# Kernel tuning notes

Measured on AMD Instinct MI355X. Metric: run time of the kernel, lower is better.

Reference implementation:

```python
import jax, jax.numpy as jnp
import numpy as np
from jax import lax

VOCAB, EMB, HID = 50000, 1024, 1024
H2 = HID // 2            # per-direction LSTM hidden
T = 4096                 # sequence length
NTAGS, START, STOP = 5, 3, 4
NEG = -10000.0


def setup_inputs() -> dict:
    key = jax.random.key(0)
    ks = jax.random.split(key, 16)
    n = lambda i, shape, s=0.05: (jax.random.normal(ks[i], shape) * s).astype(jnp.float32)
    inp = {
        "sentence": jax.random.randint(ks[0], (T,), 0, VOCAB, dtype=jnp.int64 if jax.config.jax_enable_x64 else jnp.int32),
        "h0": jax.random.normal(ks[1], (2, H2), jnp.float32),
        "c0": jax.random.normal(ks[2], (2, H2), jnp.float32),
        "embed": jax.random.normal(ks[3], (VOCAB, EMB), jnp.float32),
        "Wih_f": n(4, (4 * H2, EMB)), "Whh_f": n(5, (4 * H2, H2)),
        "bih_f": n(6, (4 * H2,)),     "bhh_f": n(7, (4 * H2,)),
        "Wih_b": n(8, (4 * H2, EMB)), "Whh_b": n(9, (4 * H2, H2)),
        "bih_b": n(10, (4 * H2,)),    "bhh_b": n(11, (4 * H2,)),
        "Wout": n(12, (NTAGS, HID)),  "bout": n(13, (NTAGS,)),
    }
    trans = jax.random.normal(ks[14], (NTAGS, NTAGS), jnp.float32)
    trans = trans.at[START, :].set(NEG).at[:, STOP].set(NEG)
    inp["trans"] = trans
    return inp


def _lstm_dir(xs, h0, c0, Wih, Whh, bih, bhh):
    # torch LSTM gate order: i, f, g, o
    def step(carry, x):
        h, c = carry
        g = Wih @ x + bih + Whh @ h + bhh
        i, f, gg, o = jnp.split(g, 4)
        c = jax.nn.sigmoid(f) * c + jax.nn.sigmoid(i) * jnp.tanh(gg)
        h = jax.nn.sigmoid(o) * jnp.tanh(c)
        return (h, c), h
    _, hs = lax.scan(step, (h0, c0), xs)
    return hs  # [T, H2]


def reference(sentence, h0, c0, embed,
              Wih_f, Whh_f, bih_f, bhh_f,
              Wih_b, Whh_b, bih_b, bhh_b,
              Wout, bout, trans):
    xs = embed[sentence]  # [T, EMB]
    hf = _lstm_dir(xs, h0[0], c0[0], Wih_f, Whh_f, bih_f, bhh_f)
    hb = _lstm_dir(xs[::-1], h0[1], c0[1], Wih_b, Whh_b, bih_b, bhh_b)[::-1]
    feats = jnp.concatenate([hf, hb], axis=-1) @ Wout.T + bout  # [T, NTAGS]

    # Viterbi decode
    fv0 = jnp.full((NTAGS,), NEG, jnp.float32).at[START].set(0.0)

    def vstep(fv, feat):
        scores = fv[None, :] + trans            # [next_tag, prev_tag]
        bp = jnp.argmax(scores, axis=1)         # best prev for each next
        fv_new = jnp.max(scores, axis=1) + feat
        return fv_new, bp

    fv, bptrs = lax.scan(vstep, fv0, feats)     # bptrs: [T, NTAGS]
    terminal = fv + trans[STOP]
    best = jnp.argmax(terminal)
    path_score = terminal[best]

    def back(tag, bp):
        prev = bp[tag]
        return prev, prev
    _, path_rev = lax.scan(back, best, bptrs[::-1])  # tags at t=T-1..0, last is START
    full = jnp.concatenate([best[None], path_rev])    # length T+1
    best_path = full[::-1][1:]                        # drop START, forward order, length T
    return path_score, best_path
```

## Files before the change

### kernel.cpp

```cpp
#include <hip/hip_runtime.h>
#include <math.h>

#define VOCAB 50000
#define EMB   1024
#define H2    512
#define R4    2048
#define TLEN  4096
#define NTAGS 5
#define STARTT 3
#define STOPT  4
#define NEGV  (-10000.0f)

#define NWG   32
#define SLICE 16

typedef unsigned long long u64;
typedef _Float16 half2v __attribute__((ext_vector_type(2)));

#define ALOAD64(p)    __hip_atomic_load((p), __ATOMIC_RELAXED, __HIP_MEMORY_SCOPE_AGENT)
#define ASTORE64(p,v) __hip_atomic_store((p), (v), __ATOMIC_RELAXED, __HIP_MEMORY_SCOPE_AGENT)

__device__ __forceinline__ float fsig(float x) {
    return __builtin_amdgcn_rcpf(1.f + __expf(-x));
}
__device__ __forceinline__ float ftanh(float x) {
    return 1.f - 2.f * __builtin_amdgcn_rcpf(1.f + __expf(2.f * x));
}

template <int CTRL>
__device__ __forceinline__ float dppadd(float x) {
    int o = __builtin_amdgcn_update_dpp(0, __float_as_int(x), CTRL, 0xf, 0xf, true);
    return x + __int_as_float(o);
}
#define RED16(a) do { \
    a = dppadd<0xB1>(a);    \
    a = dppadd<0x4E>(a);    \
    a = dppadd<0x141>(a);   \
    a = dppadd<0x128>(a);   \
} while (0)

__global__ __launch_bounds__(256) void input_gemm(
    const int* __restrict__ sent, const float* __restrict__ embed,
    const float* __restrict__ WihF, const float* __restrict__ WihB,
    const float* __restrict__ bihF, const float* __restrict__ bhhF,
    const float* __restrict__ bihB, const float* __restrict__ bhhB,
    float* __restrict__ G)
{
    __shared__ float As[32 * 64];
    __shared__ float Bs[32 * 64];
    const int tid = threadIdx.x;
    const int tm = blockIdx.x * 64;
    const int tn = blockIdx.y * 64;
    const int dir = blockIdx.z;
    const float* Wih = dir ? WihB : WihF;

    const int lr = tid >> 2;
    const int lp = tid & 3;
    const int srow = sent[tm + lr];
    const float* arow = embed + (size_t)srow * EMB;
    const float* brow = Wih + (size_t)(tn + lr) * EMB;

    const int mt = (tid & 15) * 4;
    const int nt = (tid >> 4) * 4;
    float acc[4][4] = {};

    for (int k0 = 0; k0 < EMB; k0 += 32) {
        float4 a0 = *(const float4*)(arow + k0 + lp * 8);
        float4 a1 = *(const float4*)(arow + k0 + lp * 8 + 4);
        float4 b0 = *(const float4*)(brow + k0 + lp * 8);
        float4 b1 = *(const float4*)(brow + k0 + lp * 8 + 4);
        __syncthreads();
        const int kb = lp * 8;
        As[(kb + 0) * 64 + lr] = a0.x; As[(kb + 1) * 64 + lr] = a0.y;
        As[(kb + 2) * 64 + lr] = a0.z; As[(kb + 3) * 64 + lr] = a0.w;
        As[(kb + 4) * 64 + lr] = a1.x; As[(kb + 5) * 64 + lr] = a1.y;
        As[(kb + 6) * 64 + lr] = a1.z; As[(kb + 7) * 64 + lr] = a1.w;
        Bs[(kb + 0) * 64 + lr] = b0.x; Bs[(kb + 1) * 64 + lr] = b0.y;
        Bs[(kb + 2) * 64 + lr] = b0.z; Bs[(kb + 3) * 64 + lr] = b0.w;
        Bs[(kb + 4) * 64 + lr] = b1.x; Bs[(kb + 5) * 64 + lr] = b1.y;
        Bs[(kb + 6) * 64 + lr] = b1.z; Bs[(kb + 7) * 64 + lr] = b1.w;
        __syncthreads();
        #pragma unroll
        for (int k = 0; k < 32; ++k) {
            float4 av = *(const float4*)(As + k * 64 + mt);
            float4 bv = *(const float4*)(Bs + k * 64 + nt);
            acc[0][0] += av.x * bv.x; acc[0][1] += av.x * bv.y; acc[0][2] += av.x * bv.z; acc[0][3] += av.x * bv.w;
            acc[1][0] += av.y * bv.x; acc[1][1] += av.y * bv.y; acc[1][2] += av.y * bv.z; acc[1][3] += av.y * bv.w;
            acc[2][0] += av.z * bv.x; acc[2][1] += av.z * bv.y; acc[2][2] += av.z * bv.z; acc[2][3] += av.z * bv.w;
            acc[3][0] += av.w * bv.x; acc[3][1] += av.w * bv.y; acc[3][2] += av.w * bv.z; acc[3][3] += av.w * bv.w;
        }
    }

    const float* bih = dir ? bihB : bihF;
    const float* bhh = dir ? bhhB : bhhF;
    float bias[4];
    #pragma unroll
    for (int jj = 0; jj < 4; ++jj)
        bias[jj] = bih[tn + nt + jj] + bhh[tn + nt + jj];
    float* Gd = G + (size_t)dir * TLEN * R4;
    #pragma unroll
    for (int ii = 0; ii < 4; ++ii) {
        #pragma unroll
        for (int jj = 0; jj < 4; ++jj) {
            int n = tn + nt + jj;
            int gate = n >> 9, ee = n & 511;
            Gd[(size_t)(tm + mt + ii) * R4 + ee * 4 + gate] = acc[ii][jj] + bias[jj];
        }
    }
}

__global__ __launch_bounds__(256, 1) void lstm_rec(
    const float* __restrict__ WhhF, const float* __restrict__ WhhB,
    const float* __restrict__ h0, const float* __restrict__ c0,
    const float* __restrict__ G, float* __restrict__ hs,
    u64* hbuf)
{
    const int tid  = threadIdx.x;
    const int base = blockIdx.x * SLICE;
    const int wave = tid >> 6;
    const int wl   = tid & 63;
    const int e_loc = wl >> 4;
    const int seg   = wl & 15;
    const int e     = wave * 4 + e_loc;
    const bool prod = (seg == 0);

    half2v WA[4][16], WB[4][16];
    #pragma unroll
    for (int g = 0; g < 4; ++g) {
        const float* sa = WhhF + (size_t)(g * H2 + base + e) * H2 + seg * 32;
        const float* sb = WhhB + (size_t)(g * H2 + base + e) * H2 + seg * 32;
        #pragma unroll
        for (int k = 0; k < 16; ++k) {
            half2v wa, wb;
            wa[0] = (_Float16)sa[2 * k]; wa[1] = (_Float16)sa[2 * k + 1];
            wb[0] = (_Float16)sb[2 * k]; wb[1] = (_Float16)sb[2 * k + 1];
            WA[g][k] = wa; WB[g][k] = wb;
        }
    }

    __shared__ __align__(16) unsigned hstg[2][16 * 20 + 8];

    u64* hb0 = hbuf;
    u64* hb1 = hbuf + 2 * H2;
    const int slot = tid * 2;
    const int spos = (tid >> 4) * 20 + (tid & 15);

    float cc0 = 0.f, cc1 = 0.f;
    if (prod) {
        cc0 = c0[0 * H2 + base + e];
        cc1 = c0[1 * H2 + base + e];
        ASTORE64(hb0 + base + e, ((u64)1u << 32) | __float_as_uint(h0[0 * H2 + base + e]));
        ASTORE64(hb1 + base + e, ((u64)1u << 32) | __float_as_uint(h0[1 * H2 + base + e]));
    }

    const float* G0 = G;
    const float* G1 = G + (size_t)TLEN * R4;
    float* hs0 = hs;
    float* hs1 = hs + (size_t)TLEN * H2;

    u64 p0a = ALOAD64(hb0 + slot), p0b = ALOAD64(hb0 + slot + 1);
    float4 gA = *(const float4*)(G0 + (base + e) * 4);
    float4 gB = *(const float4*)(G1 + (size_t)(TLEN - 1) * R4 + (base + e) * 4);

    #define DOT16(WARR, DBUF, A0, A1, A2, A3) do {                          \
        const uint4* Hr = (const uint4*)&hstg[DBUF][seg * 20];              \
        uint4 q0 = Hr[0], q1 = Hr[1], q2 = Hr[2], q3 = Hr[3];               \
        unsigned xs[16] = {q0.x,q0.y,q0.z,q0.w, q1.x,q1.y,q1.z,q1.w,        \
                           q2.x,q2.y,q2.z,q2.w, q3.x,q3.y,q3.z,q3.w};       \
        _Pragma("unroll")                                                   \
        for (int k = 0; k < 16; ++k) {                                      \
            half2v x = __builtin_bit_cast(half2v, xs[k]);                   \
            A0 = __builtin_amdgcn_fdot2(WARR[0][k], x, A0, false);          \
            A1 = __builtin_amdgcn_fdot2(WARR[1][k], x, A1, false);          \
            A2 = __builtin_amdgcn_fdot2(WARR[2][k], x, A2, false);          \
            A3 = __builtin_amdgcn_fdot2(WARR[3][k], x, A3, false);          \
        } } while (0)

    for (int s = 0; s < TLEN; ++s) {
        const unsigned want = (unsigned)(s + 1);
        const int rp = s & 1, wp = (s + 1) & 1;
        const int snx = (s + 1 < TLEN) ? s + 1 : s;

        while ((unsigned)(p0a >> 32) != want || (unsigned)(p0b >> 32) != want) {
            p0a = ALOAD64(hb0 + rp * H2 + slot);
            p0b = ALOAD64(hb0 + rp * H2 + slot + 1);
        }
        {
            half2v hp;
            hp[0] = (_Float16)__uint_as_float((unsigned)p0a);
            hp[1] = (_Float16)__uint_as_float((unsigned)p0b);
            hstg[0][spos] = __builtin_bit_cast(unsigned, hp);
        }
        __syncthreads();

        u64 p1a = ALOAD64(hb1 + rp * H2 + slot);
        u64 p1b = ALOAD64(hb1 + rp * H2 + slot + 1);
        float4 gAn = *(const float4*)(G0 + (size_t)snx * R4 + (base + e) * 4);

        float a0 = 0.f, a1 = 0.f, a2 = 0.f, a3 = 0.f;
        DOT16(WA, 0, a0, a1, a2, a3);
        RED16(a0); RED16(a1); RED16(a2); RED16(a3);

        if (prod) {
            float i_ = fsig(a0 + gA.x);
            float f_ = fsig(a1 + gA.y);
            float g_ = ftanh(a2 + gA.z);
            float o_ = fsig(a3 + gA.w);
            cc0 = f_ * cc0 + i_ * g_;
            float hn = o_ * ftanh(cc0);
            ASTORE64(hb0 + wp * H2 + base + e,
                     ((u64)(unsigned)(s + 2) << 32) | __float_as_uint(hn));
            hs0[(size_t)s * H2 + base + e] = hn;
        }
        gA = gAn;

        while ((unsigned)(p1a >> 32) != want || (unsigned)(p1b >> 32) != want) {
            p1a = ALOAD64(hb1 + rp * H2 + slot);
            p1b = ALOAD64(hb1 + rp * H2 + slot + 1);
        }
        {
            half2v hp;
            hp[0] = (_Float16)__uint_as_float((unsigned)p1a);
            hp[1] = (_Float16)__uint_as_float((unsigned)p1b);
            hstg[1][spos] = __builtin_bit_cast(unsigned, hp);
        }
        __syncthreads();

        p0a = ALOAD64(hb0 + wp * H2 + slot);
        p0b = ALOAD64(hb0 + wp * H2 + slot + 1);
        float4 gBn = *(const float4*)(G1 + (size_t)(TLEN - 1 - snx) * R4 + (base + e) * 4);

        float b0 = 0.f, b1 = 0.f, b2 = 0.f, b3 = 0.f;
        DOT16(WB, 1, b0, b1, b2, b3);
        RED16(b0); RED16(b1); RED16(b2); RED16(b3);

        if (prod) {
            float i_ = fsig(b0 + gB.x);
            float f_ = fsig(b1 + gB.y);
            float g_ = ftanh(b2 + gB.z);
            float o_ = fsig(b3 + gB.w);
            cc1 = f_ * cc1 + i_ * g_;
            float hn = o_ * ftanh(cc1);
            ASTORE64(hb1 + wp * H2 + base + e,
                     ((u64)(unsigned)(s + 2) << 32) | __float_as_uint(hn));
            hs1[(size_t)(TLEN - 1 - s) * H2 + base + e] = hn;
        }
        gB = gBn;
    }
    #undef DOT16
}

__global__ __launch_bounds__(64) void feat_kernel(
    const float* __restrict__ hs, const float* __restrict__ Wout,
    const float* __restrict__ bout, float* __restrict__ feats)
{
    const int t = blockIdx.x;
    const int lane = threadIdx.x;
    const float* hf = hs + (size_t)t * H2;
    const float* hb = hs + (size_t)TLEN * H2 + (size_t)t * H2;
    float x[16];
    #pragma unroll
    for (int r = 0; r < 8; ++r) x[r] = hf[lane + r * 64];
    #pragma unroll
    for (int r = 0; r < 8; ++r) x[8 + r] = hb[lane + r * 64];
    for (int j = 0; j < NTAGS; ++j) {
        const float* wr = Wout + (size_t)j * EMB;
        float p = 0.f;
        #pragma unroll
        for (int r = 0; r < 8; ++r) p += x[r] * wr[lane + r * 64];
        #pragma unroll
        for (int r = 0; r < 8; ++r) p += x[8 + r] * wr[H2 + lane + r * 64];
        #pragma unroll
        for (int off = 32; off > 0; off >>= 1) p += __shfl_down(p, off);
        if (lane == 0) feats[t * NTAGS + j] = p + bout[j];
    }
}

__global__ __launch_bounds__(64) void viterbi_kernel(
    const float* __restrict__ feats, const float* __restrict__ trans,
    float* __restrict__ out)
{
    __shared__ unsigned bp[TLEN];
    __shared__ float fch[256 * NTAGS];
    const int lane = threadIdx.x;
    const bool act = lane < 25;
    const int j = act ? (lane / 5) : 0;
    const int i = act ? (lane % 5) : 0;
    const int j5 = j * 5;
    const float tji = act ? trans[j * 5 + i] : -1e30f;
    float fv = (i == STARTT) ? 0.f : NEGV;

    for (int c0 = 0; c0 < TLEN; c0 += 256) {
        __syncthreads();
        for (int m = lane; m < 256 * NTAGS; m += 64) fch[m] = feats[c0 * NTAGS + m];
        __syncthreads();
        for (int tt = 0; tt < 256; ++tt) {
            float score = fv + tji;
            float v0 = __shfl(score, j5 + 0);
            float v1 = __shfl(score, j5 + 1);
            float v2 = __shfl(score, j5 + 2);
            float v3 = __shfl(score, j5 + 3);
            float v4 = __shfl(score, j5 + 4);
            float mm = v0; int mi = 0;
            if (v1 > mm) { mm = v1; mi = 1; }
            if (v2 > mm) { mm = v2; mi = 2; }
            if (v3 > mm) { mm = v3; mi = 3; }
            if (v4 > mm) { mm = v4; mi = 4; }
            float fnew = mm + fch[tt * NTAGS + j];
            unsigned word = ((unsigned)__shfl(mi, 0)  & 7u)
                          | (((unsigned)__shfl(mi, 5)  & 7u) << 3)
                          | (((unsigned)__shfl(mi, 10) & 7u) << 6)
                          | (((unsigned)__shfl(mi, 15) & 7u) << 9)
                          | (((unsigned)__shfl(mi, 20) & 7u) << 12);
            if (lane == 0) bp[c0 + tt] = word;
            fv = __shfl(fnew, i * 5);
        }
    }
    __syncthreads();

    float tstop = (lane < 5) ? trans[STOPT * 5 + lane] : -1e30f;
    float term = fv + tstop;
    float b0 = __shfl(term, 0), b1 = __shfl(term, 1), b2 = __shfl(term, 2);
    float b3 = __shfl(term, 3), b4 = __shfl(term, 4);
    float bsc = b0; int best = 0;
    if (b1 > bsc) { bsc = b1; best = 1; }
    if (b2 > bsc) { bsc = b2; best = 2; }
    if (b3 > bsc) { bsc = b3; best = 3; }
    if (b4 > bsc) { bsc = b4; best = 4; }

    if (lane == 0) {
        out[0] = bsc;
        int tag = best;
        out[TLEN] = (float)tag;
        #pragma unroll 16
        for (int t = TLEN - 1; t >= 1; --t) {
            tag = (int)((bp[t] >> (3 * tag)) & 7u);
            out[t] = (float)tag;
        }
    }
}

extern "C" void kernel_launch(void* const* d_in, const int* in_sizes, int n_in,
                              void* d_out, int out_size, void* d_ws, size_t ws_size,
                              hipStream_t stream) {
    const int*   sent  = (const int*)d_in[0];
    const float* h0    = (const float*)d_in[1];
    const float* c0    = (const float*)d_in[2];
    const float* embed = (const float*)d_in[3];
    const float* Wih_f = (const float*)d_in[4];
    const float* Whh_f = (const float*)d_in[5];
    const float* bih_f = (const float*)d_in[6];
    const float* bhh_f = (const float*)d_in[7];
    const float* Wih_b = (const float*)d_in[8];
    const float* Whh_b = (const float*)d_in[9];
    const float* bih_b = (const float*)d_in[10];
    const float* bhh_b = (const float*)d_in[11];
    const float* Wout  = (const float*)d_in[12];
    const float* bout  = (const float*)d_in[13];
    const float* trans = (const float*)d_in[14];

    char* ws = (char*)d_ws;
    float*    G     = (float*)(ws);
    float*    hs    = (float*)(ws + 67108864);
    u64*      hbuf  = (u64*)(ws + 83886080);
    float*    feats = (float*)(ws + 83918848);

    input_gemm<<<dim3(TLEN / 64, R4 / 64, 2), 256, 0, stream>>>(
        sent, embed, Wih_f, Wih_b, bih_f, bhh_f, bih_b, bhh_b, G);
    lstm_rec<<<NWG, 256, 0, stream>>>(Whh_f, Whh_b, h0, c0, G, hs, hbuf);
    feat_kernel<<<TLEN, 64, 0, stream>>>(hs, Wout, bout, feats);
    viterbi_kernel<<<1, 64, 0, stream>>>(feats, trans, (float*)d_out);
}
```

Measured before the change: 8.813 ms.

## Split LSTM directions across workgroups and poll packed fp16 hidden state directly

The recurrent kernel now launches 64 workgroups, one direction each, instead of 32 workgroups that alternated between both directions every step. The hidden-state mailbox now holds packed fp16 pairs with a step tag. Each lane polls its 16 slots straight from global memory and feeds them to the dot products, so the LDS staging buffer and the per-step __syncthreads are gone. The aim is to take the barrier and LDS round trip off the serial critical path and let the two directions run independently. The cost is more global polling traffic per lane and twice as many workgroups spinning at once.

```diff
diff --git a/kernel.cpp b/kernel.cpp
--- a/kernel.cpp
+++ b/kernel.cpp
@@ -10,9 +10,6 @@
 #define STARTT 3
 #define STOPT  4
 #define NEGV  (-10000.0f)
-
-#define NWG   32
-#define SLICE 16
 
 typedef unsigned long long u64;
 typedef _Float16 half2v __attribute__((ext_vector_type(2)));
@@ -109,145 +106,107 @@
     }
 }
 
-__global__ __launch_bounds__(256, 1) void lstm_rec(
+__global__ __launch_bounds__(256) void lstm_rec(
     const float* __restrict__ WhhF, const float* __restrict__ WhhB,
     const float* __restrict__ h0, const float* __restrict__ c0,
     const float* __restrict__ G, float* __restrict__ hs,
     u64* hbuf)
 {
     const int tid  = threadIdx.x;
-    const int base = blockIdx.x * SLICE;
+    const int dir  = blockIdx.x & 1;
+    const int w    = blockIdx.x >> 1;
     const int wave = tid >> 6;
     const int wl   = tid & 63;
-    const int e_loc = wl >> 4;
-    const int seg   = wl & 15;
-    const int e     = wave * 4 + e_loc;
-    const bool prod = (seg == 0);
-
-    half2v WA[4][16], WB[4][16];
+    const int r    = wl >> 4;
+    const int seg  = wl & 15;
+    const int eb   = w * 16 + wave * 4;
+    const int e    = eb + r;
+    const bool sl  = (seg == 0);
+
+    const float* Whh = dir ? WhhB : WhhF;
+
+    half2v W[4][16];
     #pragma unroll
     for (int g = 0; g < 4; ++g) {
-        const float* sa = WhhF + (size_t)(g * H2 + base + e) * H2 + seg * 32;
-        const float* sb = WhhB + (size_t)(g * H2 + base + e) * H2 + seg * 32;
+        const float* srcw = Whh + (size_t)(g * H2 + e) * H2 + seg * 32;
         #pragma unroll
         for (int k = 0; k < 16; ++k) {
-            half2v wa, wb;
-            wa[0] = (_Float16)sa[2 * k]; wa[1] = (_Float16)sa[2 * k + 1];
-            wb[0] = (_Float16)sb[2 * k]; wb[1] = (_Float16)sb[2 * k + 1];
-            WA[g][k] = wa; WB[g][k] = wb;
-        }
-    }
-
-    __shared__ __align__(16) unsigned hstg[2][16 * 20 + 8];
-
-    u64* hb0 = hbuf;
-    u64* hb1 = hbuf + 2 * H2;
-    const int slot = tid * 2;
-    const int spos = (tid >> 4) * 20 + (tid & 15);
-
-    float cc0 = 0.f, cc1 = 0.f;
-    if (prod) {
-        cc0 = c0[0 * H2 + base + e];
-        cc1 = c0[1 * H2 + base + e];
-        ASTORE64(hb0 + base + e, ((u64)1u << 32) | __float_as_uint(h0[0 * H2 + base + e]));
-        ASTORE64(hb1 + base + e, ((u64)1u << 32) | __float_as_uint(h0[1 * H2 + base + e]));
-    }
-
-    const float* G0 = G;
-    const float* G1 = G + (size_t)TLEN * R4;
-    float* hs0 = hs;
-    float* hs1 = hs + (size_t)TLEN * H2;
-
-    u64 p0a = ALOAD64(hb0 + slot), p0b = ALOAD64(hb0 + slot + 1);
-    float4 gA = *(const float4*)(G0 + (base + e) * 4);
-    float4 gB = *(const float4*)(G1 + (size_t)(TLEN - 1) * R4 + (base + e) * 4);
-
-    #define DOT16(WARR, DBUF, A0, A1, A2, A3) do {                          \
-        const uint4* Hr = (const uint4*)&hstg[DBUF][seg * 20];              \
-        uint4 q0 = Hr[0], q1 = Hr[1], q2 = Hr[2], q3 = Hr[3];               \
-        unsigned xs[16] = {q0.x,q0.y,q0.z,q0.w, q1.x,q1.y,q1.z,q1.w,        \
-                           q2.x,q2.y,q2.z,q2.w, q3.x,q3.y,q3.z,q3.w};       \
-        _Pragma("unroll")                                                   \
-        for (int k = 0; k < 16; ++k) {                                      \
-            half2v x = __builtin_bit_cast(half2v, xs[k]);                   \
-            A0 = __builtin_amdgcn_fdot2(WARR[0][k], x, A0, false);          \
-            A1 = __builtin_amdgcn_fdot2(WARR[1][k], x, A1, false);          \
-            A2 = __builtin_amdgcn_fdot2(WARR[2][k], x, A2, false);          \
-            A3 = __builtin_amdgcn_fdot2(WARR[3][k], x, A3, false);          \
-        } } while (0)
+            float2 c2 = *(const float2*)(srcw + 2 * k);
+            half2v hv; hv[0] = (_Float16)c2.x; hv[1] = (_Float16)c2.y;
+            W[g][k] = hv;
+        }
+    }
+
+    u64* mb = hbuf + (size_t)dir * 2 * 256;
+    const float* Gd = G + (size_t)dir * TLEN * R4;
+    float* hsd = hs + (size_t)dir * TLEN * H2;
+
+    float cc = 0.f;
+    if (sl) cc = c0[dir * H2 + e];
+
+    if ((wl & 31) == 0) {
+        int slot = (eb >> 1) + (wl >> 5);
+        half2v hp;
+        hp[0] = (_Float16)h0[dir * H2 + slot * 2];
+        hp[1] = (_Float16)h0[dir * H2 + slot * 2 + 1];
+        ASTORE64(mb + slot, ((u64)1u << 32) | (u64)__builtin_bit_cast(unsigned, hp));
+    }
+
+    float4 gv = make_float4(0.f, 0.f, 0.f, 0.f);
+    if (sl) gv = *(const float4*)(Gd + (size_t)(dir ? TLEN - 1 : 0) * R4 + e * 4);
 
     for (int s = 0; s < TLEN; ++s) {
+        const int t = dir ? (TLEN - 1 - s) : s;
         const unsigned want = (unsigned)(s + 1);
-        const int rp = s & 1, wp = (s + 1) & 1;
-        const int snx = (s + 1 < TLEN) ? s + 1 : s;
-
-        while ((unsigned)(p0a >> 32) != want || (unsigned)(p0b >> 32) != want) {
-            p0a = ALOAD64(hb0 + rp * H2 + slot);
-            p0b = ALOAD64(hb0 + rp * H2 + slot + 1);
-        }
-        {
-            half2v hp;
-            hp[0] = (_Float16)__uint_as_float((unsigned)p0a);
-            hp[1] = (_Float16)__uint_as_float((unsigned)p0b);
-            hstg[0][spos] = __builtin_bit_cast(unsigned, hp);
-        }
-        __syncthreads();
-
-        u64 p1a = ALOAD64(hb1 + rp * H2 + slot);
-        u64 p1b = ALOAD64(hb1 + rp * H2 + slot + 1);
-        float4 gAn = *(const float4*)(G0 + (size_t)snx * R4 + (base + e) * 4);
+        u64* src = mb + (s & 1) * 256 + seg * 16;
+
+        u64 v[16];
+        #pragma unroll
+        for (int k = 0; k < 16; ++k) v[k] = ALOAD64(src + k);
+        for (;;) {
+            unsigned bad = 0;
+            #pragma unroll
+            for (int k = 0; k < 16; ++k) bad |= ((unsigned)(v[k] >> 32)) ^ want;
+            if (bad == 0) break;
+            #pragma unroll
+            for (int k = 0; k < 16; ++k) v[k] = ALOAD64(src + k);
+        }
 
         float a0 = 0.f, a1 = 0.f, a2 = 0.f, a3 = 0.f;
-        DOT16(WA, 0, a0, a1, a2, a3);
+        #pragma unroll
+        for (int k = 0; k < 16; ++k) {
+            half2v x = __builtin_bit_cast(half2v, (unsigned)v[k]);
+            a0 = __builtin_amdgcn_fdot2(W[0][k], x, a0, false);
+            a1 = __builtin_amdgcn_fdot2(W[1][k], x, a1, false);
+            a2 = __builtin_amdgcn_fdot2(W[2][k], x, a2, false);
+            a3 = __builtin_amdgcn_fdot2(W[3][k], x, a3, false);
+        }
         RED16(a0); RED16(a1); RED16(a2); RED16(a3);
 
-        if (prod) {
-            float i_ = fsig(a0 + gA.x);
-            float f_ = fsig(a1 + gA.y);
-            float g_ = ftanh(a2 + gA.z);
-            float o_ = fsig(a3 + gA.w);
-            cc0 = f_ * cc0 + i_ * g_;
-            float hn = o_ * ftanh(cc0);
-            ASTORE64(hb0 + wp * H2 + base + e,
-                     ((u64)(unsigned)(s + 2) << 32) | __float_as_uint(hn));
-            hs0[(size_t)s * H2 + base + e] = hn;
-        }
-        gA = gAn;
-
-        while ((unsigned)(p1a >> 32) != want || (unsigned)(p1b >> 32) != want) {
-            p1a = ALOAD64(hb1 + rp * H2 + slot);
-            p1b = ALOAD64(hb1 + rp * H2 + slot + 1);
-        }
-        {
-            half2v hp;
-            hp[0] = (_Float16)__uint_as_float((unsigned)p1a);
-            hp[1] = (_Float16)__uint_as_float((unsigned)p1b);
-            hstg[1][spos] = __builtin_bit_cast(unsigned, hp);
-        }
-        __syncthreads();
-
-        p0a = ALOAD64(hb0 + wp * H2 + slot);
-        p0b = ALOAD64(hb0 + wp * H2 + slot + 1);
-        float4 gBn = *(const float4*)(G1 + (size_t)(TLEN - 1 - snx) * R4 + (base + e) * 4);
-
-        float b0 = 0.f, b1 = 0.f, b2 = 0.f, b3 = 0.f;
-        DOT16(WB, 1, b0, b1, b2, b3);
-        RED16(b0); RED16(b1); RED16(b2); RED16(b3);
-
-        if (prod) {
-            float i_ = fsig(b0 + gB.x);
-            float f_ = fsig(b1 + gB.y);
-            float g_ = ftanh(b2 + gB.z);
-            float o_ = fsig(b3 + gB.w);
-            cc1 = f_ * cc1 + i_ * g_;
-            float hn = o_ * ftanh(cc1);
-            ASTORE64(hb1 + wp * H2 + base + e,
-                     ((u64)(unsigned)(s + 2) << 32) | __float_as_uint(hn));
-            hs1[(size_t)(TLEN - 1 - s) * H2 + base + e] = hn;
-        }
-        gB = gBn;
-    }
-    #undef DOT16
+        float hn = 0.f;
+        if (sl) {
+            float i_ = fsig(a0 + gv.x);
+            float f_ = fsig(a1 + gv.y);
+            float g_ = ftanh(a2 + gv.z);
+            float o_ = fsig(a3 + gv.w);
+            cc = f_ * cc + i_ * g_;
+            hn = o_ * ftanh(cc);
+        }
+        float hpart = __shfl(hn, (wl + 16) & 63);
+        if ((wl & 31) == 0) {
+            int slot = (eb >> 1) + (wl >> 5);
+            half2v hp; hp[0] = (_Float16)hn; hp[1] = (_Float16)hpart;
+            ASTORE64(mb + ((s + 1) & 1) * 256 + slot,
+                     ((u64)(unsigned)(s + 2) << 32) | (u64)__builtin_bit_cast(unsigned, hp));
+        }
+        if (sl) {
+            hsd[(size_t)t * H2 + e] = hn;
+            if (s + 1 < TLEN) {
+                int tn2 = dir ? (TLEN - 2 - s) : (s + 1);
+                gv = *(const float4*)(Gd + (size_t)tn2 * R4 + e * 4);
+            }
+        }
+    }
 }
 
 __global__ __launch_bounds__(64) void feat_kernel(
@@ -367,7 +326,7 @@
 
     input_gemm<<<dim3(TLEN / 64, R4 / 64, 2), 256, 0, stream>>>(
         sent, embed, Wih_f, Wih_b, bih_f, bhh_f, bih_b, bhh_b, G);
-    lstm_rec<<<NWG, 256, 0, stream>>>(Whh_f, Whh_b, h0, c0, G, hs, hbuf);
+    lstm_rec<<<64, 256, 0, stream>>>(Whh_f, Whh_b, h0, c0, G, hs, hbuf);
     feat_kernel<<<TLEN, 64, 0, stream>>>(hs, Wout, bout, feats);
     viterbi_kernel<<<1, 64, 0, stream>>>(feats, trans, (float*)d_out);
 }
```

Measured after the change: 21.09 ms. 139% more time.
